# Performance work log

Hardware: AMD Instinct MI355X
Metric: run time of the kernel (lower is better)

The kernel has to match this reference:

```python
import jax, jax.numpy as jnp
import numpy as np

B, T, C, H = 1, 4096, 768, 12
D = C // H  # 64


def setup_inputs() -> dict:
    key = jax.random.key(0)
    k1, k2, k3, k4, k5 = jax.random.split(key, 5)
    x = jax.random.normal(k1, (B, T, C), dtype=jnp.float32)
    # causal mask: 1.0 where attention is DISALLOWED (strict upper triangle)
    mask = (1.0 - jnp.tril(jnp.ones((T, T), dtype=jnp.float32)))[None, None, :, :]
    s_attn = 1.0 / np.sqrt(C)
    W_qkv = jax.random.normal(k2, (C, 3 * C), dtype=jnp.float32) * s_attn
    b_qkv = jnp.zeros((3 * C,), dtype=jnp.float32)
    W_proj = jax.random.normal(k3, (C, C), dtype=jnp.float32) * s_attn
    b_proj = jnp.zeros((C,), dtype=jnp.float32)
    return {"x": x, "mask": mask, "W_qkv": W_qkv, "b_qkv": b_qkv,
            "W_proj": W_proj, "b_proj": b_proj}


def reference(x, mask, W_qkv, b_qkv, W_proj, b_proj):
    qkv = jnp.einsum('btc,cf->btf', x, W_qkv) + b_qkv        # [B,T,3C]
    q, k, v = jnp.split(qkv, 3, axis=2)
    # [B,T,C] -> [B,H,T,D]
    q = q.reshape(B, T, H, D).transpose(0, 2, 1, 3)
    k = k.reshape(B, T, H, D).transpose(0, 2, 1, 3)
    v = v.reshape(B, T, H, D).transpose(0, 2, 1, 3)
    att = jnp.einsum('bhqd,bhkd->bhqk', q, k) * (1.0 / jnp.sqrt(jnp.float32(D)))
    att = att + mask * (-1e9)
    att = jax.nn.softmax(att, axis=-1)                        # [B,H,T,T]
    y = jnp.einsum('bhqk,bhkd->bhqd', att, v)                 # [B,H,T,D]
    y = y.transpose(0, 2, 1, 3).reshape(B, T, C)
    return jnp.einsum('btc,cf->btf', y, W_proj) + b_proj
```

## Files before the change

### kernel.cpp

```cpp
#include <hip/hip_runtime.h>
#include <hip/hip_bf16.h>

typedef unsigned short u16t;
typedef short bf16x8 __attribute__((ext_vector_type(8)));
typedef short bf16x4 __attribute__((ext_vector_type(4)));
typedef float f32x4 __attribute__((ext_vector_type(4)));

#define T_SEQ 4096
#define NH    12
#define HD    64
#define C3    2304
#define CDIM  768
#define STRIP_KV 512
#define SLOTS 144
#define SC_F  0.18033688011112042f

__device__ __forceinline__ float bf2f(u16t u) {
  union { unsigned int i; float f; } c; c.i = ((unsigned int)u) << 16; return c.f;
}
__device__ __forceinline__ u16t f2bf(float f) {
  union { float f; unsigned int i; } c; c.f = f;
  unsigned int u = c.i;
  u += 0x7fffu + ((u >> 16) & 1u);
  return (u16t)(u >> 16);
}
__device__ __forceinline__ unsigned pk2bf(float a, float b) {
  __hip_bfloat162 h = __float22bfloat162_rn(make_float2(a, b));
  union { __hip_bfloat162 h; unsigned u; } c; c.h = h; return c.u;
}
__device__ __forceinline__ void gload16(const u16t* g, u16t* l) {
  __builtin_amdgcn_global_load_lds((const __attribute__((address_space(1))) void*)g,
                                   (__attribute__((address_space(3))) void*)l,
                                   16, 0, 0);
}

#define BARRIER_LGKM() __asm__ __volatile__("s_waitcnt lgkmcnt(0)\n\ts_barrier" ::: "memory")

__global__ __launch_bounds__(256) void convert_to_bf16(const float* __restrict__ in,
                                                       u16t* __restrict__ out, int n) {
  int i = blockIdx.x * 256 + threadIdx.x;
  const int stride = gridDim.x * 256;
  for (; i < n; i += stride) out[i] = f2bf(in[i]);
}

__global__ __launch_bounds__(256) void transpose_weights(const float* __restrict__ Wqkv,
                                                         const float* __restrict__ Wproj,
                                                         u16t* __restrict__ WqkvT,
                                                         u16t* __restrict__ WprojT) {
  __shared__ u16t tile[32][33];
  const int z = blockIdx.z;
  const int Cc = z ? CDIM : C3;
  if (z && blockIdx.x >= (unsigned)(CDIM / 32)) return;
  const float* in = z ? Wproj : Wqkv;
  u16t* out = z ? WprojT : WqkvT;
  const int tx = threadIdx.x, ty = threadIdx.y;
  const int c0 = blockIdx.x * 32, r0 = blockIdx.y * 32;
#pragma unroll
  for (int i = 0; i < 32; i += 8)
    tile[ty + i][tx] = f2bf(in[(size_t)(r0 + ty + i) * Cc + c0 + tx]);
  __syncthreads();
#pragma unroll
  for (int i = 0; i < 32; i += 8)
    out[(size_t)(c0 + ty + i) * CDIM + r0 + tx] = tile[tx][ty + i];
}

template <int MT, int NF, bool OUTF32>
__global__ __launch_bounds__(256) void gemm_bt_bias(
    const u16t* __restrict__ A, const u16t* __restrict__ Bt,
    const float* __restrict__ bias, void* __restrict__ Cout,
    int M, int N, int K, int qcols, float qscale) {
  constexpr int BN = 32 * NF;
  constexpr int MI = MT / 32;
  __shared__ u16t lA[MT * 32];
  __shared__ u16t lB[BN * 32];
  const int t = threadIdx.x;
  const int lane = t & 63;
  const int wid  = t >> 6;
  const int quad = lane >> 4, l16 = lane & 15;
  const int m0 = blockIdx.y * MT, n0 = blockIdx.x * BN;
  const int wm = (wid >> 1) * (16 * MI), wn = (wid & 1) * (16 * NF);

  f32x4 acc[MI][NF];
#pragma unroll
  for (int i = 0; i < MI; ++i)
#pragma unroll
    for (int j = 0; j < NF; ++j) acc[i][j] = (f32x4){0.f, 0.f, 0.f, 0.f};

  for (int k0 = 0; k0 < K; k0 += 32) {
    {
#pragma unroll
      for (int rd = 0; rd < MT / 64; ++rd) {
        const int e = rd * 256 + t;
        gload16(A + (size_t)(m0 + (e >> 2)) * K + k0 + (e & 3) * 8, &lA[e * 8]);
      }
#pragma unroll
      for (int rd = 0; rd < NF / 2; ++rd) {
        const int e = rd * 256 + t;
        gload16(Bt + (size_t)(n0 + (e >> 2)) * K + k0 + (e & 3) * 8, &lB[e * 8]);
      }
    }
    __syncthreads();
    bf16x8 af[MI], bfr[NF];
#pragma unroll
    for (int i = 0; i < MI; ++i)
      af[i] = *(const bf16x8*)&lA[(wm + i * 16 + l16) * 32 + quad * 8];
#pragma unroll
    for (int i = 0; i < NF; ++i)
      bfr[i] = *(const bf16x8*)&lB[(wn + i * 16 + l16) * 32 + quad * 8];
#pragma unroll
    for (int i = 0; i < MI; ++i)
#pragma unroll
      for (int j = 0; j < NF; ++j)
        acc[i][j] = __builtin_amdgcn_mfma_f32_16x16x32_bf16(af[i], bfr[j], acc[i][j], 0, 0, 0);
    __syncthreads();
  }

#pragma unroll
  for (int j = 0; j < NF; ++j) {
    const int col = n0 + wn + j * 16 + l16;
    const float bv = bias[col];
    const float cs = (col < qcols) ? qscale : 1.0f;
#pragma unroll
    for (int i = 0; i < MI; ++i) {
      const int rowb = m0 + wm + i * 16 + quad * 4;
#pragma unroll
      for (int r = 0; r < 4; ++r) {
        const float val = (acc[i][j][r] + bv) * cs;
        const size_t idx = (size_t)(rowb + r) * N + col;
        if (OUTF32) ((float*)Cout)[idx] = val;
        else        ((u16t*)Cout)[idx] = f2bf(val);
      }
    }
  }
}

#define KSTR 88
#define VSTR 88

__global__ __launch_bounds__(256, 4) void attn_partial(const u16t* __restrict__ qkv,
                                                       u16t* __restrict__ pO,
                                                       float* __restrict__ pL) {
  const int h     = blockIdx.x;
  const int strip = blockIdx.y;
  const int qt    = 31 - (int)blockIdx.z;
  const int q0 = qt * 128;
  const int kv_begin = strip * STRIP_KV;
  const int kv_end   = q0 + 128;
  if (kv_begin >= kv_end) return;
  const int kv_stop = (kv_begin + STRIP_KV < kv_end) ? kv_begin + STRIP_KV : kv_end;
  const int a = qt >> 2, b = qt & 3;
  const int slot = (a + 1) * (2 * a + b) + strip;

  __shared__ u16t lK[64 * KSTR];
  __shared__ u16t lVt[64 * VSTR];

  const int t = threadIdx.x;
  const int lane = t & 63;
  const int wid  = t >> 6;
  const int quad = lane >> 4, l16 = lane & 15;
  const int wr = q0 + wid * 32;

  const int krow = t >> 3, kcol = (t & 7) * 8;
  const int vk0 = 4 * (t >> 4);
  const int vd0 = 4 * (t & 15);
  const int vswz = (t & 3) << 3;
  const u16t* Kbase = qkv + CDIM + h * HD;
  const u16t* Vbase = qkv + 2 * CDIM + h * HD;

  bf16x8 qf[2][2];
#pragma unroll
  for (int qn = 0; qn < 2; ++qn) {
    const int row = wr + qn * 16 + l16;
#pragma unroll
    for (int kd = 0; kd < 2; ++kd)
      qf[qn][kd] = *(const bf16x8*)(qkv + (size_t)row * C3 + h * HD + kd * 32 + quad * 8);
  }

  f32x4 oaccT[4][2];
  f32x4 laccT[2];
#pragma unroll
  for (int dn = 0; dn < 4; ++dn)
#pragma unroll
    for (int qn = 0; qn < 2; ++qn) oaccT[dn][qn] = (f32x4){0.f, 0.f, 0.f, 0.f};
#pragma unroll
  for (int qn = 0; qn < 2; ++qn) laccT[qn] = (f32x4){0.f, 0.f, 0.f, 0.f};
  bf16x4 ones4;
#pragma unroll
  for (int i = 0; i < 4; ++i) ones4[i] = (short)0x3F80;

  const int pswz = ((l16 >> 2) & 3) << 3;

  uint4 kreg0, kreg1;
  union { uint2 u; u16t hw[4]; } vreg[4];

#define LOAD_TILE(KV0)                                                        \
  do {                                                                        \
    kreg0 = *(const uint4*)(Kbase + (size_t)((KV0) + krow) * C3 + kcol);      \
    kreg1 = *(const uint4*)(Kbase + (size_t)((KV0) + krow + 32) * C3 + kcol); \
    _Pragma("unroll")                                                         \
    for (int i = 0; i < 4; ++i)                                               \
      vreg[i].u = *(const uint2*)(Vbase + (size_t)((KV0) + vk0 + i) * C3 + vd0); \
  } while (0)

#define STORE_TILE()                                                          \
  do {                                                                        \
    *(uint4*)&lK[krow * KSTR + kcol] = kreg0;                                 \
    *(uint4*)&lK[(krow + 32) * KSTR + kcol] = kreg1;                          \
    _Pragma("unroll")                                                         \
    for (int j = 0; j < 4; ++j) {                                             \
      union { uint2 u; u16t hw[4]; } w;                                       \
      w.hw[0] = vreg[0].hw[j]; w.hw[1] = vreg[1].hw[j];                       \
      w.hw[2] = vreg[2].hw[j]; w.hw[3] = vreg[3].hw[j];                       \
      *(uint2*)&lVt[(vd0 + j) * VSTR + (vk0 ^ vswz)] = w.u;                   \
    }                                                                         \
  } while (0)

  LOAD_TILE(kv_begin);
  STORE_TILE();

  for (int kv0 = kv_begin; kv0 < kv_stop; kv0 += 64) {
    const bool havenext = (kv0 + 64 < kv_stop);
    if (havenext) LOAD_TILE(kv0 + 64);
    BARRIER_LGKM();

    if (kv0 <= wr + 31) {
      f32x4 sacc[4][2];
#pragma unroll
      for (int kvt = 0; kvt < 4; ++kvt) {
        bf16x8 kf0 = *(const bf16x8*)&lK[(kvt * 16 + l16) * KSTR + quad * 8];
        bf16x8 kf1 = *(const bf16x8*)&lK[(kvt * 16 + l16) * KSTR + 32 + quad * 8];
#pragma unroll
        for (int qn = 0; qn < 2; ++qn) {
          f32x4 s = (f32x4){0.f, 0.f, 0.f, 0.f};
          s = __builtin_amdgcn_mfma_f32_16x16x32_bf16(kf0, qf[qn][0], s, 0, 0, 0);
          s = __builtin_amdgcn_mfma_f32_16x16x32_bf16(kf1, qf[qn][1], s, 0, 0, 0);
          sacc[kvt][qn] = s;
        }
      }
      const bool need_mask = (kv0 + 63 > wr);
      bf16x4 pbf[4][2];
#pragma unroll
      for (int kvt = 0; kvt < 4; ++kvt)
#pragma unroll
        for (int qn = 0; qn < 2; ++qn) {
          const int qg = wr + qn * 16 + l16;
          float pv[4];
#pragma unroll
          for (int r = 0; r < 4; ++r) {
            const int kvg = kv0 + kvt * 16 + quad * 4 + r;
            float p = __builtin_amdgcn_exp2f(sacc[kvt][qn][r]);
            if (need_mask && (kvg > qg)) p = 0.f;
            pv[r] = p;
          }
          union { bf16x4 v; unsigned u[2]; } pw;
          pw.u[0] = pk2bf(pv[0], pv[1]);
          pw.u[1] = pk2bf(pv[2], pv[3]);
          pbf[kvt][qn] = pw.v;
        }
#pragma unroll
      for (int kvt = 0; kvt < 4; ++kvt) {
        const int kvcol = (kvt * 16 + quad * 4) ^ pswz;
#pragma unroll
        for (int qn = 0; qn < 2; ++qn)
          laccT[qn] = __builtin_amdgcn_mfma_f32_16x16x16bf16_1k(
              ones4, pbf[kvt][qn], laccT[qn], 0, 0, 0);
#pragma unroll
        for (int dn = 0; dn < 4; ++dn) {
          bf16x4 vf = *(const bf16x4*)&lVt[(dn * 16 + l16) * VSTR + kvcol];
#pragma unroll
          for (int qn = 0; qn < 2; ++qn)
            oaccT[dn][qn] = __builtin_amdgcn_mfma_f32_16x16x16bf16_1k(
                vf, pbf[kvt][qn], oaccT[dn][qn], 0, 0, 0);
        }
      }
    }
    BARRIER_LGKM();
    if (havenext) STORE_TILE();
  }

  {
    u16t* scr = &lVt[wid * 16 * 80];
    u16t* po = pO + ((size_t)h * SLOTS + slot) * 128 * HD;
    float* pl = pL + ((size_t)h * SLOTS + slot) * 128;
#pragma unroll
    for (int qn = 0; qn < 2; ++qn) {
#pragma unroll
      for (int dn = 0; dn < 4; ++dn) {
        union { bf16x4 v; unsigned u[2]; } w;
        w.u[0] = pk2bf(oaccT[dn][qn][0], oaccT[dn][qn][1]);
        w.u[1] = pk2bf(oaccT[dn][qn][2], oaccT[dn][qn][3]);
        *(bf16x4*)&scr[l16 * 80 + dn * 16 + quad * 4] = w.v;
      }
      __asm__ __volatile__("s_waitcnt lgkmcnt(0)" ::: "memory");
      const int ql = wid * 32 + qn * 16 + l16;
      uint4 w0 = *(const uint4*)&scr[l16 * 80 + quad * 16];
      uint4 w1 = *(const uint4*)&scr[l16 * 80 + quad * 16 + 8];
      u16t* dst = po + (size_t)ql * HD + quad * 16;
      *(uint4*)dst = w0;
      *(uint4*)(dst + 8) = w1;
      if (quad == 0) pl[ql] = laccT[qn][0];
      __asm__ __volatile__("s_waitcnt lgkmcnt(0)" ::: "memory");
    }
  }
#undef LOAD_TILE
#undef STORE_TILE
}

__global__ __launch_bounds__(256) void attn_normalize(const u16t* __restrict__ pO,
                                                      const float* __restrict__ pL,
                                                      u16t* __restrict__ y) {
  const int i = blockIdx.x * 256 + threadIdx.x;
  const int q = i / (CDIM / 4), c4 = (i % (CDIM / 4)) * 4;
  const int h = c4 >> 6, d = c4 & 63;
  const int qt = q >> 7, ql = q & 127;
  const int a = qt >> 2, b = qt & 3;
  const int base = (a + 1) * (2 * a + b);
  const int ns = a + 1;
  float o0 = 0.f, o1 = 0.f, o2 = 0.f, o3 = 0.f, l = 0.f;
  for (int s = 0; s < ns; ++s) {
    const size_t sl = (size_t)h * SLOTS + base + s;
    union { uint2 u; u16t hw[4]; } v;
    v.u = *(const uint2*)&pO[(sl * 128 + ql) * HD + d];
    o0 += bf2f(v.hw[0]); o1 += bf2f(v.hw[1]);
    o2 += bf2f(v.hw[2]); o3 += bf2f(v.hw[3]);
    l += pL[sl * 128 + ql];
  }
  const float rl = 1.0f / l;
  union { uint2 u; unsigned w[2]; } wv;
  wv.w[0] = pk2bf(o0 * rl, o1 * rl);
  wv.w[1] = pk2bf(o2 * rl, o3 * rl);
  *(uint2*)&y[(size_t)q * CDIM + c4] = wv.u;
}

extern "C" void kernel_launch(void* const* d_in, const int* in_sizes, int n_in,
                              void* d_out, int out_size, void* d_ws, size_t ws_size,
                              hipStream_t stream) {
  const float* x     = (const float*)d_in[0];
  const float* Wqkv  = (const float*)d_in[2];
  const float* bqkv  = (const float*)d_in[3];
  const float* Wproj = (const float*)d_in[4];
  const float* bproj = (const float*)d_in[5];

  u16t* qkv    = (u16t*)d_ws;
  u16t* ybuf   = qkv    + (size_t)T_SEQ * C3;
  u16t* WqkvT  = ybuf   + (size_t)T_SEQ * CDIM;
  u16t* WprojT = WqkvT  + (size_t)C3 * CDIM;
  u16t* pO     = WprojT + (size_t)CDIM * CDIM;
  float* pL    = (float*)(pO + (size_t)NH * SLOTS * 128 * HD);

  convert_to_bf16<<<1024, 256, 0, stream>>>(x, ybuf, T_SEQ * CDIM);
  transpose_weights<<<dim3(C3 / 32, CDIM / 32, 2), dim3(32, 8), 0, stream>>>(
      Wqkv, Wproj, WqkvT, WprojT);
  gemm_bt_bias<128, 4, false><<<dim3(C3 / 128, T_SEQ / 128), 256, 0, stream>>>(
      ybuf, WqkvT, bqkv, qkv, T_SEQ, C3, CDIM, CDIM, SC_F);
  attn_partial<<<dim3(NH, 8, T_SEQ / 128), 256, 0, stream>>>(qkv, pO, pL);
  attn_normalize<<<(T_SEQ * CDIM / 4) / 256, 256, 0, stream>>>(pO, pL, ybuf);
  gemm_bt_bias<64, 2, true><<<dim3(CDIM / 64, T_SEQ / 64), 256, 0, stream>>>(
      ybuf, WprojT, bproj, d_out, T_SEQ, CDIM, CDIM, 0, 1.0f);
}
```

Measured before the change: 227.3 us.

## Fuse x bf16 conversion into QKV GEMM and register-prefetch GEMM tiles

Removes the separate fp32-to-bf16 conversion kernel for x by having the QKV GEMM load fp32 A tiles directly and convert them while staging into LDS. The GEMM loop is restructured from direct global-to-LDS loads into a register prefetch of the next k-tile that overlaps the MFMA work, with LDS stores after the second barrier. The normalize kernel is widened to 8 elements per thread. In exchange it uses more registers for the prefetch buffers, doubles the A read bandwidth in fp32, and drops the async LDS-load path.

```diff
diff --git a/kernel.cpp b/kernel.cpp
--- a/kernel.cpp
+++ b/kernel.cpp
@@ -28,20 +28,8 @@
   __hip_bfloat162 h = __float22bfloat162_rn(make_float2(a, b));
   union { __hip_bfloat162 h; unsigned u; } c; c.h = h; return c.u;
 }
-__device__ __forceinline__ void gload16(const u16t* g, u16t* l) {
-  __builtin_amdgcn_global_load_lds((const __attribute__((address_space(1))) void*)g,
-                                   (__attribute__((address_space(3))) void*)l,
-                                   16, 0, 0);
-}
 
 #define BARRIER_LGKM() __asm__ __volatile__("s_waitcnt lgkmcnt(0)\n\ts_barrier" ::: "memory")
-
-__global__ __launch_bounds__(256) void convert_to_bf16(const float* __restrict__ in,
-                                                       u16t* __restrict__ out, int n) {
-  int i = blockIdx.x * 256 + threadIdx.x;
-  const int stride = gridDim.x * 256;
-  for (; i < n; i += stride) out[i] = f2bf(in[i]);
-}
 
 __global__ __launch_bounds__(256) void transpose_weights(const float* __restrict__ Wqkv,
                                                          const float* __restrict__ Wproj,
@@ -64,13 +52,15 @@
     out[(size_t)(c0 + ty + i) * CDIM + r0 + tx] = tile[tx][ty + i];
 }
 
-template <int MT, int NF, bool OUTF32>
+template <int MT, int NF, bool AF32, bool OUTF32>
 __global__ __launch_bounds__(256) void gemm_bt_bias(
-    const u16t* __restrict__ A, const u16t* __restrict__ Bt,
+    const void* __restrict__ Ain, const u16t* __restrict__ Bt,
     const float* __restrict__ bias, void* __restrict__ Cout,
     int M, int N, int K, int qcols, float qscale) {
   constexpr int BN = 32 * NF;
   constexpr int MI = MT / 32;
+  constexpr int AR = MT / 64;
+  constexpr int BR = NF / 2;
   __shared__ u16t lA[MT * 32];
   __shared__ u16t lB[BN * 32];
   const int t = threadIdx.x;
@@ -86,20 +76,57 @@
 #pragma unroll
     for (int j = 0; j < NF; ++j) acc[i][j] = (f32x4){0.f, 0.f, 0.f, 0.f};
 
+  uint4 pa[AR * 2], pb[BR];
+
+#define GLOADK(K0)                                                            \
+  do {                                                                        \
+    _Pragma("unroll")                                                         \
+    for (int rd = 0; rd < AR; ++rd) {                                         \
+      const int e = rd * 256 + t;                                             \
+      const int row = m0 + (e >> 2), col = (K0) + (e & 3) * 8;                \
+      if (AF32) {                                                             \
+        const float* ap = (const float*)Ain + (size_t)row * K + col;          \
+        pa[rd * 2]     = *(const uint4*)ap;                                   \
+        pa[rd * 2 + 1] = *(const uint4*)(ap + 4);                             \
+      } else {                                                                \
+        pa[rd * 2] = *(const uint4*)((const u16t*)Ain + (size_t)row * K + col); \
+      }                                                                       \
+    }                                                                         \
+    _Pragma("unroll")                                                         \
+    for (int rd = 0; rd < BR; ++rd) {                                         \
+      const int e = rd * 256 + t;                                             \
+      pb[rd] = *(const uint4*)(Bt + (size_t)(n0 + (e >> 2)) * K + (K0) + (e & 3) * 8); \
+    }                                                                         \
+  } while (0)
+
+#define STOREK()                                                              \
+  do {                                                                        \
+    _Pragma("unroll")                                                         \
+    for (int rd = 0; rd < AR; ++rd) {                                         \
+      const int e = rd * 256 + t;                                             \
+      if (AF32) {                                                             \
+        union { uint4 u; float f[4]; } a0, a1;                                \
+        a0.u = pa[rd * 2]; a1.u = pa[rd * 2 + 1];                             \
+        union { uint4 u; unsigned w[4]; } o;                                  \
+        o.w[0] = pk2bf(a0.f[0], a0.f[1]); o.w[1] = pk2bf(a0.f[2], a0.f[3]);   \
+        o.w[2] = pk2bf(a1.f[0], a1.f[1]); o.w[3] = pk2bf(a1.f[2], a1.f[3]);   \
+        *(uint4*)&lA[e * 8] = o.u;                                            \
+      } else {                                                                \
+        *(uint4*)&lA[e * 8] = pa[rd * 2];                                     \
+      }                                                                       \
+    }                                                                         \
+    _Pragma("unroll")                                                         \
+    for (int rd = 0; rd < BR; ++rd)                                           \
+      *(uint4*)&lB[(rd * 256 + t) * 8] = pb[rd];                              \
+  } while (0)
+
+  GLOADK(0);
+  STOREK();
+
   for (int k0 = 0; k0 < K; k0 += 32) {
-    {
-#pragma unroll
-      for (int rd = 0; rd < MT / 64; ++rd) {
-        const int e = rd * 256 + t;
-        gload16(A + (size_t)(m0 + (e >> 2)) * K + k0 + (e & 3) * 8, &lA[e * 8]);
-      }
-#pragma unroll
-      for (int rd = 0; rd < NF / 2; ++rd) {
-        const int e = rd * 256 + t;
-        gload16(Bt + (size_t)(n0 + (e >> 2)) * K + k0 + (e & 3) * 8, &lB[e * 8]);
-      }
-    }
-    __syncthreads();
+    const bool hn = (k0 + 32 < K);
+    if (hn) GLOADK(k0 + 32);
+    BARRIER_LGKM();
     bf16x8 af[MI], bfr[NF];
 #pragma unroll
     for (int i = 0; i < MI; ++i)
@@ -112,7 +139,8 @@
 #pragma unroll
       for (int j = 0; j < NF; ++j)
         acc[i][j] = __builtin_amdgcn_mfma_f32_16x16x32_bf16(af[i], bfr[j], acc[i][j], 0, 0, 0);
-    __syncthreads();
+    BARRIER_LGKM();
+    if (hn) STOREK();
   }
 
 #pragma unroll
@@ -132,6 +160,8 @@
       }
     }
   }
+#undef GLOADK
+#undef STOREK
 }
 
 #define KSTR 88
@@ -310,26 +340,28 @@
                                                       const float* __restrict__ pL,
                                                       u16t* __restrict__ y) {
   const int i = blockIdx.x * 256 + threadIdx.x;
-  const int q = i / (CDIM / 4), c4 = (i % (CDIM / 4)) * 4;
-  const int h = c4 >> 6, d = c4 & 63;
+  const int q = i / (CDIM / 8), c8 = (i % (CDIM / 8)) * 8;
+  const int h = c8 >> 6, d = c8 & 63;
   const int qt = q >> 7, ql = q & 127;
   const int a = qt >> 2, b = qt & 3;
   const int base = (a + 1) * (2 * a + b);
   const int ns = a + 1;
-  float o0 = 0.f, o1 = 0.f, o2 = 0.f, o3 = 0.f, l = 0.f;
+  float o[8] = {0.f, 0.f, 0.f, 0.f, 0.f, 0.f, 0.f, 0.f};
+  float l = 0.f;
   for (int s = 0; s < ns; ++s) {
     const size_t sl = (size_t)h * SLOTS + base + s;
-    union { uint2 u; u16t hw[4]; } v;
-    v.u = *(const uint2*)&pO[(sl * 128 + ql) * HD + d];
-    o0 += bf2f(v.hw[0]); o1 += bf2f(v.hw[1]);
-    o2 += bf2f(v.hw[2]); o3 += bf2f(v.hw[3]);
+    union { uint4 u; u16t hw[8]; } v;
+    v.u = *(const uint4*)&pO[(sl * 128 + ql) * HD + d];
+#pragma unroll
+    for (int j = 0; j < 8; ++j) o[j] += bf2f(v.hw[j]);
     l += pL[sl * 128 + ql];
   }
   const float rl = 1.0f / l;
-  union { uint2 u; unsigned w[2]; } wv;
-  wv.w[0] = pk2bf(o0 * rl, o1 * rl);
-  wv.w[1] = pk2bf(o2 * rl, o3 * rl);
-  *(uint2*)&y[(size_t)q * CDIM + c4] = wv.u;
+  union { uint4 u; unsigned w[4]; } wv;
+#pragma unroll
+  for (int j = 0; j < 4; ++j)
+    wv.w[j] = pk2bf(o[2 * j] * rl, o[2 * j + 1] * rl);
+  *(uint4*)&y[(size_t)q * CDIM + c8] = wv.u;
 }
 
 extern "C" void kernel_launch(void* const* d_in, const int* in_sizes, int n_in,
@@ -348,13 +380,12 @@
   u16t* pO     = WprojT + (size_t)CDIM * CDIM;
   float* pL    = (float*)(pO + (size_t)NH * SLOTS * 128 * HD);
 
-  convert_to_bf16<<<1024, 256, 0, stream>>>(x, ybuf, T_SEQ * CDIM);
   transpose_weights<<<dim3(C3 / 32, CDIM / 32, 2), dim3(32, 8), 0, stream>>>(
       Wqkv, Wproj, WqkvT, WprojT);
-  gemm_bt_bias<128, 4, false><<<dim3(C3 / 128, T_SEQ / 128), 256, 0, stream>>>(
-      ybuf, WqkvT, bqkv, qkv, T_SEQ, C3, CDIM, CDIM, SC_F);
+  gemm_bt_bias<128, 4, true, false><<<dim3(C3 / 128, T_SEQ / 128), 256, 0, stream>>>(
+      x, WqkvT, bqkv, qkv, T_SEQ, C3, CDIM, CDIM, SC_F);
   attn_partial<<<dim3(NH, 8, T_SEQ / 128), 256, 0, stream>>>(qkv, pO, pL);
-  attn_normalize<<<(T_SEQ * CDIM / 4) / 256, 256, 0, stream>>>(pO, pL, ybuf);
-  gemm_bt_bias<64, 2, true><<<dim3(CDIM / 64, T_SEQ / 64), 256, 0, stream>>>(
+  attn_normalize<<<(T_SEQ * CDIM / 8) / 256, 256, 0, stream>>>(pO, pL, ybuf);
+  gemm_bt_bias<64, 2, false, true><<<dim3(CDIM / 64, T_SEQ / 64), 256, 0, stream>>>(
       ybuf, WprojT, bproj, d_out, T_SEQ, CDIM, CDIM, 0, 1.0f);
 }
```

New measurement: 307.4 us. 1.35x slower.
